# Kernel optimization log

Measured on AMD Instinct MI355X. Metric: run time of the kernel, lower is better.

Reference implementation:

```python
import jax, jax.numpy as jnp
import numpy as np

B, S, H, W = 256, 512, 1024, 64  # batch, seq, hidden_dim, context_window

def setup_inputs() -> dict:
    key = jax.random.key(0)
    k1, k2, k3, k4, k5, k6 = jax.random.split(key, 6)
    inputs = jax.random.normal(k1, (B, S, H), jnp.float32)
    # lengths must be >= context_window and <= S
    setence_len = W + jax.random.randint(k2, (B,), 0, S - W + 1)
    # parent < W <= len ensures len - parent - 1 >= 0 (valid index)
    parent = jax.random.randint(k3, (B,), 0, W)
    hc = jax.random.normal(k4, (B, H), jnp.float32)
    # nn.Linear(2H, H) params
    W_attn = jax.random.normal(k5, (H, 2 * H), jnp.float32) * (1.0 / np.sqrt(2 * H))
    b_attn = jnp.zeros((H,), jnp.float32)
    # nn.Parameter(torch.rand(H)) -> uniform [0,1)
    v = jax.random.uniform(k6, (H,), jnp.float32)
    return {"inputs": inputs, "hc": hc, "W_attn": W_attn, "b_attn": b_attn,
            "v": v, "setence_len": setence_len, "parent": parent}

def reference(inputs, hc, W_attn, b_attn, v, setence_len, parent):
    # Mt: per-sample window inputs[b, len_b-W:len_b, :] -> [B, W, H]
    idx = setence_len[:, None] - W + jnp.arange(W)[None, :]          # [B, W]
    Mt = jnp.take_along_axis(inputs, idx[:, :, None], axis=1)        # [B, W, H]
    # par: inputs[b, len_b - parent_b - 1, :] -> [B, H]
    pidx = (setence_len - parent - 1)[:, None, None]                 # [B, 1, 1]
    par = jnp.take_along_axis(inputs, pidx, axis=1)[:, 0, :]         # [B, H]
    # h = hc repeated over the window axis -> [B, W, H]
    h = jnp.broadcast_to(hc[:, None, :], Mt.shape)
    # additive (Bahdanau) scoring
    energy = jnp.tanh(jnp.concatenate([h, Mt], axis=-1) @ W_attn.T + b_attn)  # [B, W, H]
    scores = jnp.einsum('h,bwh->bw', v, energy)                      # [B, W]
    attn = jax.nn.softmax(scores, axis=-1)                           # [B, W]
    attn_weights = attn[:, None, :]                                  # [B, 1, W]
    context = jnp.einsum('bw,bwh->bh', attn, Mt)[:, None, :]         # [B, 1, H]
    return attn_weights, context, par
```

## Files before the change

### kernel.cpp

```cpp
#include <hip/hip_runtime.h>
#include <math.h>

#define Bdim 256
#define Sdim 512
#define Hdim 1024
#define Wdim 64
#define BK 32
#define JTILE 256
#define NJT 4
#define MTILE 128
#define KC 4

#define WS_SCORES_F (NJT * Bdim * Wdim)
#define WS_NEED_BYTES ((size_t)(WS_SCORES_F + KC * Bdim * Hdim) * 4)

#define ASTRIDE 140
#define AS_F (BK * ASTRIDE)
#define SMEM_F (AS_F + BK * JTILE)
#define HC0_OFF 0
#define HCW_OFF 2048
#define VS_OFF  2560

__global__ __launch_bounds__(256) void k_hcw(
    const float* __restrict__ hc, const float* __restrict__ Wa,
    float* __restrict__ part)
{
  const int jt = blockIdx.x, bt = blockIdx.y, kc = blockIdx.z;
  const int t = threadIdx.x;
  const int b0 = bt * 16;
  const int kb = kc * 256;
  __shared__ float As[BK][20];
  __shared__ float Bs[BK][256];
  const int tb = t & 3, tj = t >> 2;
  float acc[4][4] = {{0.f}};
  const float* brow = Wa + (size_t)(jt * 256 + t) * (2 * Hdim) + kb;
  const int r = t & 15, kq = t >> 4;
  for (int k0 = 0; k0 < 256; k0 += BK) {
    float4 bld[8];
    #pragma unroll
    for (int q = 0; q < 8; ++q) bld[q] = *(const float4*)(brow + k0 + q * 4);
    float4 ald = make_float4(0.f, 0.f, 0.f, 0.f);
    if (t < 128) ald = *(const float4*)(hc + (size_t)(b0 + r) * Hdim + kb + k0 + kq * 4);
    __syncthreads();
    #pragma unroll
    for (int q = 0; q < 8; ++q)
      #pragma unroll
      for (int e = 0; e < 4; ++e)
        Bs[q * 4 + e][t] = ((const float*)&bld[q])[e];
    if (t < 128) {
      #pragma unroll
      for (int e = 0; e < 4; ++e) As[kq * 4 + e][r] = ((const float*)&ald)[e];
    }
    __syncthreads();
    #pragma unroll 8
    for (int k = 0; k < BK; ++k) {
      const float4 av = *(const float4*)&As[k][tb * 4];
      const float4 bv = *(const float4*)&Bs[k][tj * 4];
      const float A4[4] = {av.x, av.y, av.z, av.w};
      const float B4[4] = {bv.x, bv.y, bv.z, bv.w};
      #pragma unroll
      for (int i = 0; i < 4; ++i)
        #pragma unroll
        for (int jj = 0; jj < 4; ++jj)
          acc[i][jj] = fmaf(A4[i], B4[jj], acc[i][jj]);
    }
  }
  float* outp = part + (size_t)kc * (Bdim * Hdim);
  #pragma unroll
  for (int i = 0; i < 4; ++i)
    #pragma unroll
    for (int jj = 0; jj < 4; ++jj)
      outp[(size_t)(b0 + tb * 4 + i) * Hdim + jt * 256 + tj * 4 + jj] = acc[i][jj];
}

template<int USE_PART>
__global__ __launch_bounds__(256, 2) void k_scores(
    const float* __restrict__ inputs, const float* __restrict__ hc,
    const float* __restrict__ Wa, const float* __restrict__ ba,
    const float* __restrict__ v, const int* __restrict__ slen,
    float* __restrict__ ws_scores, const float* __restrict__ part)
{
  const int jt = blockIdx.x;
  const int b0 = blockIdx.y * 2;
  const int t = threadIdx.x;
  __shared__ float smem[SMEM_F];
  float* Bsb = smem + AS_F;

  const int tw = t & 15, tj = t >> 4;
  const int w0 = tw * 8, j0 = tj * 16;
  const int awp = w0 + 4 * (tw >> 2);

  const int ar = t >> 1, ah = t & 1;
  const int absub = ar >> 6;
  const int slA = slen[b0 + absub];
  const float* arow = inputs +
      ((size_t)(b0 + absub) * Sdim + slA - Wdim + (ar & 63)) * Hdim + ah * 16;
  const int aphys = ar + 4 * (ar >> 5);
  const float* brow = Wa + (size_t)(jt * JTILE + t) * (2 * Hdim) + Hdim;

  float acc[8][16];
  #pragma unroll
  for (int i = 0; i < 8; ++i)
    #pragma unroll
    for (int jj = 0; jj < 16; ++jj) acc[i][jj] = 0.f;

  for (int k0 = 0; k0 < Hdim; k0 += BK) {
    float4 a_ld[4];
    #pragma unroll
    for (int c = 0; c < 4; ++c) a_ld[c] = *(const float4*)(arow + k0 + c * 4);
    float4 b_ld[8];
    #pragma unroll
    for (int q = 0; q < 8; ++q) b_ld[q] = *(const float4*)(brow + k0 + q * 4);
    __syncthreads();
    #pragma unroll
    for (int c = 0; c < 4; ++c)
      #pragma unroll
      for (int e = 0; e < 4; ++e)
        smem[(ah * 16 + c * 4 + e) * ASTRIDE + aphys] = ((const float*)&a_ld[c])[e];
    #pragma unroll
    for (int q = 0; q < 8; ++q)
      #pragma unroll
      for (int e = 0; e < 4; ++e)
        Bsb[(q * 4 + e) * JTILE + t] = ((const float*)&b_ld[q])[e];
    __syncthreads();
    #pragma unroll 8
    for (int k = 0; k < BK; ++k) {
      const float* Ak = smem + k * ASTRIDE;
      const float* Bk = Bsb + k * JTILE;
      const float4 av0 = *(const float4*)(Ak + awp);
      const float4 av1 = *(const float4*)(Ak + awp + 4);
      const float4 bv0 = *(const float4*)(Bk + j0);
      const float4 bv1 = *(const float4*)(Bk + j0 + 4);
      const float4 bv2 = *(const float4*)(Bk + j0 + 8);
      const float4 bv3 = *(const float4*)(Bk + j0 + 12);
      const float A8[8]  = {av0.x, av0.y, av0.z, av0.w, av1.x, av1.y, av1.z, av1.w};
      const float B16[16] = {bv0.x, bv0.y, bv0.z, bv0.w, bv1.x, bv1.y, bv1.z, bv1.w,
                             bv2.x, bv2.y, bv2.z, bv2.w, bv3.x, bv3.y, bv3.z, bv3.w};
      #pragma unroll
      for (int wi = 0; wi < 8; ++wi)
        #pragma unroll
        for (int ji = 0; ji < 16; ++ji)
          acc[wi][ji] = fmaf(A8[wi], B16[ji], acc[wi][ji]);
    }
  }

  __syncthreads();

  const int j = jt * JTILE + t;
  if (USE_PART) {
    float h0 = ba[j], h1 = ba[j];
    #pragma unroll
    for (int kc = 0; kc < KC; ++kc) {
      h0 += part[(size_t)kc * (Bdim * Hdim) + (size_t)b0 * Hdim + j];
      h1 += part[(size_t)kc * (Bdim * Hdim) + (size_t)(b0 + 1) * Hdim + j];
    }
    smem[HCW_OFF + t] = h0;
    smem[HCW_OFF + 256 + t] = h1;
    smem[VS_OFF + t] = v[j];
  } else {
    for (int i = t; i < 2 * Hdim; i += 256) smem[HC0_OFF + i] = hc[(size_t)b0 * Hdim + i];
    __syncthreads();
    const float* w1row = Wa + (size_t)j * (2 * Hdim);
    float s0 = 0.f, s1 = 0.f;
    #pragma unroll 4
    for (int k = 0; k < Hdim; k += 4) {
      const float4 wv  = *(const float4*)(w1row + k);
      const float4 h0v = *(const float4*)(smem + HC0_OFF + k);
      const float4 h1v = *(const float4*)(smem + HC0_OFF + Hdim + k);
      s0 = fmaf(wv.x, h0v.x, s0); s0 = fmaf(wv.y, h0v.y, s0);
      s0 = fmaf(wv.z, h0v.z, s0); s0 = fmaf(wv.w, h0v.w, s0);
      s1 = fmaf(wv.x, h1v.x, s1); s1 = fmaf(wv.y, h1v.y, s1);
      s1 = fmaf(wv.z, h1v.z, s1); s1 = fmaf(wv.w, h1v.w, s1);
    }
    __syncthreads();
    smem[HCW_OFF + t] = s0 + ba[j];
    smem[HCW_OFF + 256 + t] = s1 + ba[j];
    smem[VS_OFF + t] = v[j];
  }
  __syncthreads();

  const int bsub = tw >> 3;
  float sloc[8] = {0.f, 0.f, 0.f, 0.f, 0.f, 0.f, 0.f, 0.f};
  #pragma unroll
  for (int ji = 0; ji < 16; ++ji) {
    const float hw = smem[HCW_OFF + bsub * 256 + j0 + ji];
    const float vj = smem[VS_OFF + j0 + ji];
    #pragma unroll
    for (int wi = 0; wi < 8; ++wi)
      sloc[wi] = fmaf(vj, tanhf(acc[wi][ji] + hw), sloc[wi]);
  }
  float* red = smem + AS_F;
  #pragma unroll
  for (int wi = 0; wi < 8; ++wi) red[tj * MTILE + w0 + wi] = sloc[wi];
  __syncthreads();
  if (t < MTILE) {
    float s = 0.f;
    #pragma unroll
    for (int p = 0; p < 16; ++p) s += red[p * MTILE + t];
    ws_scores[(size_t)jt * (Bdim * Wdim) + (size_t)(b0 + (t >> 6)) * Wdim + (t & 63)] = s;
  }
}

__global__ __launch_bounds__(256) void k_finish(
    const float* __restrict__ inputs, const int* __restrict__ slen,
    const int* __restrict__ parent, const float* __restrict__ ws_scores,
    float* __restrict__ out)
{
  const int b = blockIdx.x;
  const int c = blockIdx.y;
  const int t = threadIdx.x;
  const int sl = slen[b];
  __shared__ float attn[64];

  if (t < 64) {
    float s = ws_scores[b * Wdim + t]
            + ws_scores[1 * (Bdim * Wdim) + b * Wdim + t]
            + ws_scores[2 * (Bdim * Wdim) + b * Wdim + t]
            + ws_scores[3 * (Bdim * Wdim) + b * Wdim + t];
    float mx = s;
    #pragma unroll
    for (int off = 32; off > 0; off >>= 1) mx = fmaxf(mx, __shfl_xor(mx, off));
    const float e = __expf(s - mx);
    float sm = e;
    #pragma unroll
    for (int off = 32; off > 0; off >>= 1) sm += __shfl_xor(sm, off);
    const float a = e / sm;
    if (c == 0) out[b * Wdim + t] = a;
    attn[t] = a;
  }
  __syncthreads();

  const float* base = inputs + ((size_t)b * Sdim + sl - Wdim) * Hdim + c * 256;
  float a0 = 0.f;
  #pragma unroll 8
  for (int w = 0; w < Wdim; ++w)
    a0 = fmaf(attn[w], base[(size_t)w * Hdim + t], a0);
  out[Bdim * Wdim + (size_t)b * Hdim + c * 256 + t] = a0;

  const float* pr = inputs + ((size_t)b * Sdim + sl - parent[b] - 1) * Hdim + c * 256;
  out[Bdim * Wdim + Bdim * Hdim + (size_t)b * Hdim + c * 256 + t] = pr[t];
}

extern "C" void kernel_launch(void* const* d_in, const int* in_sizes, int n_in,
                              void* d_out, int out_size, void* d_ws, size_t ws_size,
                              hipStream_t stream) {
  const float* inputs = (const float*)d_in[0];
  const float* hc     = (const float*)d_in[1];
  const float* Wa     = (const float*)d_in[2];
  const float* ba     = (const float*)d_in[3];
  const float* v      = (const float*)d_in[4];
  const int*   slen   = (const int*)d_in[5];
  const int*   parent = (const int*)d_in[6];
  float* out = (float*)d_out;
  float* ws  = (float*)d_ws;

  const bool use_part = (ws_size >= WS_NEED_BYTES);
  if (use_part) {
    k_hcw<<<dim3(NJT, 16, KC), 256, 0, stream>>>(hc, Wa, ws + WS_SCORES_F);
    k_scores<1><<<dim3(NJT, Bdim / 2), 256, 0, stream>>>(
        inputs, hc, Wa, ba, v, slen, ws, ws + WS_SCORES_F);
  } else {
    k_scores<0><<<dim3(NJT, Bdim / 2), 256, 0, stream>>>(
        inputs, hc, Wa, ba, v, slen, ws, nullptr);
  }
  k_finish<<<dim3(Bdim, 4), 256, 0, stream>>>(inputs, slen, parent, ws, out);
}
```

Measured before the change: 995.3 us.

## Compute Mt·W2 scores with split-bf16 MFMA instead of FP32 FMA

Adds a kernel that splits the Mt-side weight half into high and low bf16 parts, plus a new scores kernel. The new kernel splits the windowed activations the same way on the fly and accumulates hi*hi + lo*hi + hi*lo with 16x16x32 bf16 MFMA instructions, using swizzled LDS tiles and a register prefetch of the next K chunk. The aim is to move the dominant GEMM from scalar FP32 FMAs onto matrix cores while keeping near-FP32 accuracy through the three-term split. It costs an extra weight conversion kernel each call and more workspace, and drops the lo*lo term, so precision is slightly reduced.

```diff
diff --git a/kernel.cpp b/kernel.cpp
--- a/kernel.cpp
+++ b/kernel.cpp
@@ -11,8 +11,14 @@
 #define MTILE 128
 #define KC 4
 
+typedef __attribute__((ext_vector_type(8))) short bf16x8;
+typedef __attribute__((ext_vector_type(4))) float f32x4;
+
 #define WS_SCORES_F (NJT * Bdim * Wdim)
-#define WS_NEED_BYTES ((size_t)(WS_SCORES_F + KC * Bdim * Hdim) * 4)
+#define WS_PART_F   (KC * Bdim * Hdim)
+#define WS_WSP_F    (Hdim * Hdim / 2)
+#define WS_NEED_BYTES  ((size_t)(WS_SCORES_F + WS_PART_F) * 4)
+#define WS_MFMA_BYTES  ((size_t)(WS_SCORES_F + WS_PART_F + WS_WSP_F) * 4)
 
 #define ASTRIDE 140
 #define AS_F (BK * ASTRIDE)
@@ -20,6 +26,32 @@
 #define HC0_OFF 0
 #define HCW_OFF 2048
 #define VS_OFF  2560
+
+__device__ __forceinline__ unsigned pk2(unsigned short a, unsigned short b) {
+  return (unsigned)a | ((unsigned)b << 16);
+}
+
+__global__ __launch_bounds__(256) void k_wsplit(
+    const float* __restrict__ Wa, unsigned short* __restrict__ wsp)
+{
+  const int j = blockIdx.x;
+  const int t = threadIdx.x;
+  const float4 xv = *(const float4*)(Wa + (size_t)j * (2 * Hdim) + Hdim + 4 * t);
+  unsigned short h[4], l[4];
+  #pragma unroll
+  for (int e = 0; e < 4; ++e) {
+    const float x = ((const float*)&xv)[e];
+    const unsigned u = __float_as_uint(x);
+    const float hif = __uint_as_float(u & 0xFFFF0000u);
+    const float lof = x - hif;
+    h[e] = (unsigned short)(u >> 16);
+    l[e] = (unsigned short)(__float_as_uint(lof) >> 16);
+  }
+  const int kc = (4 * t) >> 5, ki = (4 * t) & 31;
+  unsigned short* base = wsp + (size_t)j * 2048 + kc * 64 + ki;
+  *(ushort4*)(base)      = make_ushort4(h[0], h[1], h[2], h[3]);
+  *(ushort4*)(base + 32) = make_ushort4(l[0], l[1], l[2], l[3]);
+}
 
 __global__ __launch_bounds__(256) void k_hcw(
     const float* __restrict__ hc, const float* __restrict__ Wa,
@@ -73,6 +105,175 @@
       outp[(size_t)(b0 + tb * 4 + i) * Hdim + jt * 256 + tj * 4 + jj] = acc[i][jj];
 }
 
+__global__ __launch_bounds__(512) void k_scores_mfma(
+    const float* __restrict__ inputs, const float* __restrict__ ba,
+    const float* __restrict__ v, const int* __restrict__ slen,
+    float* __restrict__ ws_scores, const float* __restrict__ part,
+    const unsigned short* __restrict__ wsp)
+{
+  const int jt = blockIdx.x;
+  const int b0 = blockIdx.y * 4;
+  const int t = threadIdx.x;
+  const int lane = t & 63, wv = t >> 6, wm = wv >> 1, wn = wv & 1;
+
+  __shared__ uint4 lds4[65536 / 16];
+  char* As = (char*)lds4;
+  char* Bs = (char*)lds4 + 32768;
+
+  const int ar = t >> 1, ah = t & 1;
+  const int ab = ar >> 6;
+  const int slA = slen[b0 + ab];
+  const float* aptr = inputs +
+      ((size_t)(b0 + ab) * Sdim + slA - Wdim + (ar & 63)) * Hdim + ah * 16;
+  const int arw = ar & 7;
+  char* aw0 = As + ar * 128;
+  const int bj = t >> 1, bc = t & 1;
+  const unsigned short* bptr = wsp + (size_t)(jt * 256 + bj) * 2048 + bc * 32;
+  const int bjw = bj & 7;
+  char* bw0 = Bs + bj * 128;
+
+  int aoff[4][2], boff[8][2];
+  #pragma unroll
+  for (int mt = 0; mt < 4; ++mt) {
+    const int row = wm * 64 + mt * 16 + (lane & 15);
+    const int s0 = lane >> 4;
+    aoff[mt][0] = row * 128 + ((s0 ^ (row & 7)) << 4);
+    aoff[mt][1] = row * 128 + (((s0 + 4) ^ (row & 7)) << 4);
+  }
+  #pragma unroll
+  for (int nt = 0; nt < 8; ++nt) {
+    const int row = wn * 128 + nt * 16 + (lane & 15);
+    const int s0 = lane >> 4;
+    boff[nt][0] = row * 128 + ((s0 ^ (row & 7)) << 4);
+    boff[nt][1] = row * 128 + (((s0 + 4) ^ (row & 7)) << 4);
+  }
+
+  f32x4 acc[4][8];
+  #pragma unroll
+  for (int mt = 0; mt < 4; ++mt)
+    #pragma unroll
+    for (int nt = 0; nt < 8; ++nt) {
+      f32x4 z = {0.f, 0.f, 0.f, 0.f};
+      acc[mt][nt] = z;
+    }
+
+  float4 a_ld[4];
+  uint4  b_ld[4];
+  #pragma unroll
+  for (int c = 0; c < 4; ++c) a_ld[c] = *(const float4*)(aptr + c * 4);
+  #pragma unroll
+  for (int q = 0; q < 4; ++q) b_ld[q] = *(const uint4*)(bptr + q * 8);
+
+  for (int k0 = 0; k0 < Hdim; k0 += 32) {
+    __syncthreads();
+    unsigned short h[16], l[16];
+    #pragma unroll
+    for (int c = 0; c < 4; ++c)
+      #pragma unroll
+      for (int e = 0; e < 4; ++e) {
+        const float x = ((const float*)&a_ld[c])[e];
+        const unsigned u = __float_as_uint(x);
+        const float hif = __uint_as_float(u & 0xFFFF0000u);
+        const float lof = x - hif;
+        h[c * 4 + e] = (unsigned short)(u >> 16);
+        l[c * 4 + e] = (unsigned short)(__float_as_uint(lof) >> 16);
+      }
+    uint4 H0 = make_uint4(pk2(h[0], h[1]), pk2(h[2], h[3]), pk2(h[4], h[5]), pk2(h[6], h[7]));
+    uint4 H1 = make_uint4(pk2(h[8], h[9]), pk2(h[10], h[11]), pk2(h[12], h[13]), pk2(h[14], h[15]));
+    uint4 L0 = make_uint4(pk2(l[0], l[1]), pk2(l[2], l[3]), pk2(l[4], l[5]), pk2(l[6], l[7]));
+    uint4 L1 = make_uint4(pk2(l[8], l[9]), pk2(l[10], l[11]), pk2(l[12], l[13]), pk2(l[14], l[15]));
+    *(uint4*)(aw0 + (((2 * ah + 0) ^ arw) << 4)) = H0;
+    *(uint4*)(aw0 + (((2 * ah + 1) ^ arw) << 4)) = H1;
+    *(uint4*)(aw0 + (((4 + 2 * ah + 0) ^ arw) << 4)) = L0;
+    *(uint4*)(aw0 + (((4 + 2 * ah + 1) ^ arw) << 4)) = L1;
+    #pragma unroll
+    for (int q = 0; q < 4; ++q)
+      *(uint4*)(bw0 + (((bc * 4 + q) ^ bjw) << 4)) = b_ld[q];
+    if (k0 + 32 < Hdim) {
+      #pragma unroll
+      for (int c = 0; c < 4; ++c) a_ld[c] = *(const float4*)(aptr + k0 + 32 + c * 4);
+      const int kc = (k0 + 32) >> 5;
+      #pragma unroll
+      for (int q = 0; q < 4; ++q) b_ld[q] = *(const uint4*)(bptr + kc * 64 + q * 8);
+    }
+    __syncthreads();
+    bf16x8 ahf[4], alf[4];
+    #pragma unroll
+    for (int mt = 0; mt < 4; ++mt) {
+      ahf[mt] = *(const bf16x8*)(As + aoff[mt][0]);
+      alf[mt] = *(const bf16x8*)(As + aoff[mt][1]);
+    }
+    #pragma unroll
+    for (int nt = 0; nt < 8; ++nt) {
+      const bf16x8 bh = *(const bf16x8*)(Bs + boff[nt][0]);
+      const bf16x8 bl = *(const bf16x8*)(Bs + boff[nt][1]);
+      #pragma unroll
+      for (int mt = 0; mt < 4; ++mt) {
+        acc[mt][nt] = __builtin_amdgcn_mfma_f32_16x16x32_bf16(ahf[mt], bh, acc[mt][nt], 0, 0, 0);
+        acc[mt][nt] = __builtin_amdgcn_mfma_f32_16x16x32_bf16(alf[mt], bh, acc[mt][nt], 0, 0, 0);
+        acc[mt][nt] = __builtin_amdgcn_mfma_f32_16x16x32_bf16(ahf[mt], bl, acc[mt][nt], 0, 0, 0);
+      }
+    }
+  }
+
+  __syncthreads();
+  float* scr   = (float*)lds4;
+  float* hcw_s = scr;
+  float* v_s   = scr + 1024;
+  float* red   = scr + 1280;
+  for (int idx = t; idx < 1024; idx += 512) {
+    const int bb = idx >> 8, jj = idx & 255;
+    const int jg = jt * 256 + jj;
+    float s = ba[jg];
+    #pragma unroll
+    for (int kc = 0; kc < KC; ++kc)
+      s += part[(size_t)kc * (Bdim * Hdim) + (size_t)(b0 + bb) * Hdim + jg];
+    hcw_s[idx] = s;
+  }
+  if (t < 256) v_s[t] = v[jt * 256 + t];
+  __syncthreads();
+
+  float sred[4][4];
+  #pragma unroll
+  for (int mt = 0; mt < 4; ++mt)
+    #pragma unroll
+    for (int r = 0; r < 4; ++r) sred[mt][r] = 0.f;
+  #pragma unroll
+  for (int nt = 0; nt < 8; ++nt) {
+    const int col = wn * 128 + nt * 16 + (lane & 15);
+    const float hw0 = hcw_s[wm * 256 + col];
+    const float vj = v_s[col];
+    #pragma unroll
+    for (int mt = 0; mt < 4; ++mt)
+      #pragma unroll
+      for (int r = 0; r < 4; ++r) {
+        const float s = ((const float*)&acc[mt][nt])[r] + hw0;
+        sred[mt][r] = fmaf(vj, tanhf(s), sred[mt][r]);
+      }
+  }
+  #pragma unroll
+  for (int mt = 0; mt < 4; ++mt)
+    #pragma unroll
+    for (int r = 0; r < 4; ++r) {
+      float x = sred[mt][r];
+      x += __shfl_xor(x, 1); x += __shfl_xor(x, 2);
+      x += __shfl_xor(x, 4); x += __shfl_xor(x, 8);
+      sred[mt][r] = x;
+    }
+  if ((lane & 15) == 0) {
+    #pragma unroll
+    for (int mt = 0; mt < 4; ++mt)
+      #pragma unroll
+      for (int r = 0; r < 4; ++r)
+        red[wn * 256 + wm * 64 + mt * 16 + (lane >> 4) * 4 + r] = sred[mt][r];
+  }
+  __syncthreads();
+  if (t < 256) {
+    const float s = red[t] + red[256 + t];
+    ws_scores[(size_t)jt * (Bdim * Wdim) + (size_t)(b0 + (t >> 6)) * Wdim + (t & 63)] = s;
+  }
+}
+
 template<int USE_PART>
 __global__ __launch_bounds__(256, 2) void k_scores(
     const float* __restrict__ inputs, const float* __restrict__ hc,
@@ -145,7 +346,6 @@
   }
 
   __syncthreads();
-
   const int j = jt * JTILE + t;
   if (USE_PART) {
     float h0 = ba[j], h1 = ba[j];
@@ -253,12 +453,18 @@
   const int*   parent = (const int*)d_in[6];
   float* out = (float*)d_out;
   float* ws  = (float*)d_ws;
-
-  const bool use_part = (ws_size >= WS_NEED_BYTES);
-  if (use_part) {
-    k_hcw<<<dim3(NJT, 16, KC), 256, 0, stream>>>(hc, Wa, ws + WS_SCORES_F);
+  float* part = ws + WS_SCORES_F;
+  unsigned short* wsp = (unsigned short*)(ws + WS_SCORES_F + WS_PART_F);
+
+  if (ws_size >= WS_MFMA_BYTES) {
+    k_wsplit<<<dim3(Hdim), 256, 0, stream>>>(Wa, wsp);
+    k_hcw<<<dim3(NJT, 16, KC), 256, 0, stream>>>(hc, Wa, part);
+    k_scores_mfma<<<dim3(NJT, Bdim / 4), 512, 0, stream>>>(
+        inputs, ba, v, slen, ws, part, wsp);
+  } else if (ws_size >= WS_NEED_BYTES) {
+    k_hcw<<<dim3(NJT, 16, KC), 256, 0, stream>>>(hc, Wa, part);
     k_scores<1><<<dim3(NJT, Bdim / 2), 256, 0, stream>>>(
-        inputs, hc, Wa, ba, v, slen, ws, ws + WS_SCORES_F);
+        inputs, hc, Wa, ba, v, slen, ws, part);
   } else {
     k_scores<0><<<dim3(NJT, Bdim / 2), 256, 0, stream>>>(
         inputs, hc, Wa, ba, v, slen, ws, nullptr);
```

Measured after the change: 818.2 us. -17.8%, faster.
